# Optimization experiments

Measured on AMD Instinct MI355X. Metric: run time of the kernel, lower is better.

The kernel has to match this reference:

```python
import jax, jax.numpy as jnp
import numpy as np

N_HEADS = 16
EPS = 1e-5

def _ln(h, g, b):
    mu = jnp.mean(h, axis=-1, keepdims=True)
    var = jnp.var(h, axis=-1, keepdims=True)
    return (h - mu) * jax.lax.rsqrt(var + EPS) * g + b

def setup_inputs() -> dict:
    key = jax.random.key(0)
    ks = jax.random.split(key, 8)
    B, S, D, M = 2, 2048, 2048, 8192
    x = jax.random.normal(ks[0], (B, S, D), dtype=jnp.float32)
    # causal mask: True where attention is disallowed (j > i)
    mask = jnp.triu(jnp.ones((S, S), dtype=bool), k=1)[None, None]
    s = 1.0 / np.sqrt(D)
    Wq = jax.random.normal(ks[1], (D, D), dtype=jnp.float32) * s
    Wk = jax.random.normal(ks[2], (D, D), dtype=jnp.float32) * s
    Wv = jax.random.normal(ks[3], (D, D), dtype=jnp.float32) * s
    Wo = jax.random.normal(ks[4], (D, D), dtype=jnp.float32) * s
    W1 = jax.random.normal(ks[5], (D, M), dtype=jnp.float32) * s
    b1 = jnp.zeros((M,), dtype=jnp.float32)
    W2 = jax.random.normal(ks[6], (M, D), dtype=jnp.float32) * (1.0 / np.sqrt(M))
    b2 = jnp.zeros((D,), dtype=jnp.float32)
    ln1_g = jnp.ones((D,), jnp.float32); ln1_b = jnp.zeros((D,), jnp.float32)
    ln2_g = jnp.ones((D,), jnp.float32); ln2_b = jnp.zeros((D,), jnp.float32)
    return dict(x=x, self_attn_mask=mask, Wq=Wq, Wk=Wk, Wv=Wv, Wo=Wo,
                ln1_g=ln1_g, ln1_b=ln1_b, W1=W1, b1=b1, W2=W2, b2=b2,
                ln2_g=ln2_g, ln2_b=ln2_b)

def reference(x, self_attn_mask, Wq, Wk, Wv, Wo, ln1_g, ln1_b, W1, b1, W2, b2, ln2_g, ln2_b):
    B, S, D = x.shape
    n = N_HEADS
    d = D // n
    # --- self-attention with pre-norm residual ---
    h = _ln(x, ln1_g, ln1_b)
    # NOTE: source uses .view(b, n_heads, i, head_dim) with NO transpose -> plain reshape
    q = (h @ Wq).reshape(B, n, S, d)
    k = (h @ Wk).reshape(B, n, S, d)
    v = (h @ Wv).reshape(B, n, S, d)
    score = jnp.einsum('bnid,bnjd->bnij', q, k)
    # NOTE: source masks BEFORE scaling, so -1e9 is also divided by sqrt(d)
    score = jnp.where(self_attn_mask, jnp.float32(-1e9), score) / jnp.sqrt(jnp.float32(d))
    w = jax.nn.softmax(score, axis=3)
    o = jnp.einsum('bnij,bnjd->bnid', w, v)
    o = o.transpose(0, 2, 1, 3).reshape(B, S, D)  # b n i d -> b i (n d)
    x = x + o @ Wo
    # --- FFN with pre-norm residual ---
    h2 = _ln(x, ln2_g, ln2_b)
    ff = jnp.maximum(h2 @ W1 + b1, 0.0) @ W2 + b2
    return x + ff
```

## Files before the change

### kernel.cpp

```cpp
#include <hip/hip_runtime.h>
#include <cstdint>

using bf16x8 = __attribute__((ext_vector_type(8))) short;
using f32x4  = __attribute__((ext_vector_type(4))) float;

__device__ __forceinline__ unsigned short f2bf(float f) {
  union { float f; unsigned u; } v; v.f = f;
  unsigned u = v.u;
  u += 0x7fffu + ((u >> 16) & 1u);
  return (unsigned short)(u >> 16);
}

__global__ __launch_bounds__(256) void ln_kernel(
    const float* __restrict__ x, const float* __restrict__ g,
    const float* __restrict__ bb, unsigned short* __restrict__ h)
{
  const int D = 2048;
  const int row = blockIdx.x;
  const float* xr = x + (size_t)row * D;
  const int t = threadIdx.x;
  float4 v0 = ((const float4*)xr)[t];
  float4 v1 = ((const float4*)xr)[t + 256];
  float s  = v0.x+v0.y+v0.z+v0.w + v1.x+v1.y+v1.z+v1.w;
  float ss = v0.x*v0.x+v0.y*v0.y+v0.z*v0.z+v0.w*v0.w
           + v1.x*v1.x+v1.y*v1.y+v1.z*v1.z+v1.w*v1.w;
  #pragma unroll
  for (int off = 1; off < 64; off <<= 1) {
    s  += __shfl_xor(s, off);
    ss += __shfl_xor(ss, off);
  }
  __shared__ float red[8];
  const int wave = t >> 6, lane = t & 63;
  if (lane == 0) { red[wave] = s; red[4+wave] = ss; }
  __syncthreads();
  s  = red[0]+red[1]+red[2]+red[3];
  ss = red[4]+red[5]+red[6]+red[7];
  const float mu   = s * (1.f/2048.f);
  const float var  = ss * (1.f/2048.f) - mu*mu;
  const float rstd = rsqrtf(var + 1e-5f);
  unsigned short* hr = h + (size_t)row * D;
  #pragma unroll
  for (int q = 0; q < 2; ++q) {
    float4 v = q ? v1 : v0;
    int vecidx = t + q*256;
    float4 gg  = ((const float4*)g)[vecidx];
    float4 bv  = ((const float4*)bb)[vecidx];
    ushort4 o;
    o.x = f2bf((v.x-mu)*rstd*gg.x + bv.x);
    o.y = f2bf((v.y-mu)*rstd*gg.y + bv.y);
    o.z = f2bf((v.z-mu)*rstd*gg.z + bv.z);
    o.w = f2bf((v.w-mu)*rstd*gg.w + bv.w);
    *(ushort4*)(hr + vecidx*4) = o;
  }
}

__global__ __launch_bounds__(256) void transpose_cast(
    const float* __restrict__ W, unsigned short* __restrict__ WT,
    int K, int N)
{
  __shared__ float tile[32][33];
  const int tx = threadIdx.x, ty = threadIdx.y;
  const int n0 = blockIdx.x * 32, k0 = blockIdx.y * 32;
  #pragma unroll
  for (int r = 0; r < 4; ++r)
    tile[ty + r*8][tx] = W[(size_t)(k0 + ty + r*8) * N + n0 + tx];
  __syncthreads();
  #pragma unroll
  for (int r = 0; r < 4; ++r)
    WT[(size_t)(n0 + ty + r*8) * K + k0 + tx] = f2bf(tile[tx][ty + r*8]);
}

template<bool BIAS, bool RELU, bool RESID, bool OUTBF16>
__global__ __launch_bounds__(256, 2) void gemm_bt(
    const unsigned short* __restrict__ A, const unsigned short* __restrict__ BT,
    const float* __restrict__ bias, const float* __restrict__ resid,
    void* __restrict__ Cp, int M, int N, int K)
{
  constexpr int BM = 128, BN = 128, BK = 64, PK = 72;
  __shared__ __align__(16) unsigned short As[BM*PK];
  __shared__ __align__(16) unsigned short Bs[BN*PK];
  const int tid  = threadIdx.x;
  const int lane = tid & 63;
  const int wave = tid >> 6;
  const int l15 = lane & 15, lh = lane >> 4;
  const size_t bm = (size_t)blockIdx.y * BM, bn = (size_t)blockIdx.x * BN;
  const int wm = (wave >> 1) * 64, wn = (wave & 1) * 64;
  f32x4 acc[4][4] = {};
  bf16x8 ar[4], br[4];
  const int nk = K / BK;

  auto loadG = [&](int kt) {
    #pragma unroll
    for (int q = 0; q < 4; ++q) {
      int c = tid + q*256;
      int row = c >> 3, k0 = (c & 7) * 8;
      ar[q] = *(const bf16x8*)(A  + (bm + row)*(size_t)K + (size_t)kt*BK + k0);
      br[q] = *(const bf16x8*)(BT + (bn + row)*(size_t)K + (size_t)kt*BK + k0);
    }
  };
  loadG(0);
  for (int kt = 0; kt < nk; ++kt) {
    __syncthreads();
    #pragma unroll
    for (int q = 0; q < 4; ++q) {
      int c = tid + q*256;
      int row = c >> 3, k0 = (c & 7) * 8;
      *(bf16x8*)(&As[row*PK + k0]) = ar[q];
      *(bf16x8*)(&Bs[row*PK + k0]) = br[q];
    }
    __syncthreads();
    if (kt + 1 < nk) loadG(kt + 1);
    #pragma unroll
    for (int kk = 0; kk < 2; ++kk) {
      bf16x8 af[4], bfr[4];
      #pragma unroll
      for (int i = 0; i < 4; ++i) {
        af[i]  = *(const bf16x8*)(&As[(wm + i*16 + l15)*PK + kk*32 + lh*8]);
        bfr[i] = *(const bf16x8*)(&Bs[(wn + i*16 + l15)*PK + kk*32 + lh*8]);
      }
      #pragma unroll
      for (int i = 0; i < 4; ++i)
        #pragma unroll
        for (int j = 0; j < 4; ++j)
          acc[i][j] = __builtin_amdgcn_mfma_f32_16x16x32_bf16(af[i], bfr[j], acc[i][j], 0, 0, 0);
    }
  }
  float bv[4];
  if (BIAS) {
    #pragma unroll
    for (int j = 0; j < 4; ++j) bv[j] = bias[bn + wn + j*16 + l15];
  }
  #pragma unroll
  for (int i = 0; i < 4; ++i) {
    #pragma unroll
    for (int r = 0; r < 4; ++r) {
      size_t rrow = bm + wm + i*16 + lh*4 + r;
      #pragma unroll
      for (int j = 0; j < 4; ++j) {
        size_t ccol = bn + wn + j*16 + l15;
        float v = acc[i][j][r];
        if (BIAS)  v += bv[j];
        if (RELU)  v = fmaxf(v, 0.f);
        if (RESID) v += resid[rrow*(size_t)N + ccol];
        if (OUTBF16) ((unsigned short*)Cp)[rrow*(size_t)N + ccol] = f2bf(v);
        else         ((float*)Cp)[rrow*(size_t)N + ccol] = v;
      }
    }
  }
}

__global__ __launch_bounds__(256) void attn_kernel(
    const unsigned short* __restrict__ QKV, unsigned short* __restrict__ O)
{
  constexpr float SCALE = 0.08838834764831845f;
  __shared__ __align__(16) unsigned short Kl[64*128];
  __shared__ __align__(16) unsigned short Vf[64*128];
  __shared__ __align__(16) unsigned short Pl[4*1024];
  const int bid = blockIdx.x;
  const int qt = 31 - (bid >> 5);
  const int nh = bid & 15;
  const int b  = (bid >> 4) & 1;
  const int t = threadIdx.x;
  const int lane = t & 63, wave = t >> 6;
  const int l15 = lane & 15, lh = lane >> 4;
  const int i0 = qt*64 + wave*16;
  const size_t RS = 6144;
  const size_t base = (size_t)b * 2048 * RS;

  const unsigned short* qrow = QKV + base + (size_t)(nh*128 + (i0 >> 4)) * RS;
  bf16x8 qf[4];
  #pragma unroll
  for (int c = 0; c < 4; ++c)
    qf[c] = *(const bf16x8*)(qrow + l15*128 + c*32 + lh*8);

  f32x4 of[8] = {};
  float mrun[4], lrun[4];
  #pragma unroll
  for (int r = 0; r < 4; ++r) { mrun[r] = -INFINITY; lrun[r] = 0.f; }

  const int nkt = qt + 1;
  bf16x8 kr[4], vr[4];
  auto loadKV = [&](int kt) {
    #pragma unroll
    for (int q = 0; q < 4; ++q) {
      int c = t + q*256;
      int j = c >> 4, dd0 = (c & 15) * 8;
      const size_t grow = base + (size_t)(nh*128 + kt*4 + (j >> 4)) * RS + (j & 15)*128 + dd0;
      kr[q] = *(const bf16x8*)(QKV + grow + 2048);
      vr[q] = *(const bf16x8*)(QKV + grow + 4096);
    }
  };
  loadKV(0);

  for (int kt = 0; kt < nkt; ++kt) {
    __syncthreads();
    #pragma unroll
    for (int q = 0; q < 4; ++q) {
      int c = t + q*256;
      int j = c >> 4, dd0 = (c & 15) * 8;
      *(bf16x8*)((char*)Kl + ((j*256 + dd0*2) ^ ((j & 7) << 4))) = kr[q];
      int ks = j >> 5, jq = j & 31;
      int cc = dd0 >> 4;
      int wb = ks*8192 + cc*1024 + (((dd0 & 15) + 16*((jq >> 3) & 3)) & ~7)*16 + (jq & 7)*2;
      #pragma unroll
      for (int e = 0; e < 8; ++e)
        *(unsigned short*)((char*)Vf + wb + ((e ^ cc) * 16)) = (unsigned short)vr[q][e];
    }
    __syncthreads();
    if (kt + 1 < nkt) loadKV(kt + 1);

    f32x4 sc[4] = {};
    #pragma unroll
    for (int jt = 0; jt < 4; ++jt) {
      int row = jt*16 + l15;
      const char* kb = (const char*)Kl + row*256;
      const int sw = (row & 7) << 4;
      #pragma unroll
      for (int c = 0; c < 4; ++c) {
        bf16x8 kf = *(const bf16x8*)(kb + ((c*64 + lh*16) ^ sw));
        sc[jt] = __builtin_amdgcn_mfma_f32_16x16x32_bf16(qf[c], kf, sc[jt], 0, 0, 0);
      }
    }

    float fac[4];
    char* pw = (char*)Pl + wave*2048;
    #pragma unroll
    for (int r = 0; r < 4; ++r) {
      float s0 = sc[0][r]*SCALE, s1 = sc[1][r]*SCALE, s2 = sc[2][r]*SCALE, s3 = sc[3][r]*SCALE;
      if (kt == qt) {
        const int i = i0 + lh*4 + r;
        const int j = kt*64 + l15;
        s0 = (j      > i) ? -INFINITY : s0;
        s1 = (j + 16 > i) ? -INFINITY : s1;
        s2 = (j + 32 > i) ? -INFINITY : s2;
        s3 = (j + 48 > i) ? -INFINITY : s3;
      }
      float mx = fmaxf(fmaxf(s0, s1), fmaxf(s2, s3));
      #pragma unroll
      for (int mk = 1; mk < 16; mk <<= 1) mx = fmaxf(mx, __shfl_xor(mx, mk));
      const float mnew = fmaxf(mrun[r], mx);
      float p0 = __expf(s0 - mnew), p1 = __expf(s1 - mnew);
      float p2 = __expf(s2 - mnew), p3 = __expf(s3 - mnew);
      float psum = (p0 + p1) + (p2 + p3);
      #pragma unroll
      for (int mk = 1; mk < 16; mk <<= 1) psum += __shfl_xor(psum, mk);
      fac[r]  = __expf(mrun[r] - mnew);
      lrun[r] = lrun[r]*fac[r] + psum;
      mrun[r] = mnew;
      const int io = lh*4 + r;
      const int swp = (io & 7) << 4;
      char* pr = pw + io*128;
      *(unsigned short*)(pr + ((     l15*2) ^ swp)) = f2bf(p0);
      *(unsigned short*)(pr + ((32 + l15*2) ^ swp)) = f2bf(p1);
      *(unsigned short*)(pr + ((64 + l15*2) ^ swp)) = f2bf(p2);
      *(unsigned short*)(pr + ((96 + l15*2) ^ swp)) = f2bf(p3);
    }
    #pragma unroll
    for (int c = 0; c < 8; ++c)
      #pragma unroll
      for (int r = 0; r < 4; ++r)
        of[c][r] *= fac[r];

    const char* prd = pw + l15*128;
    const int psw = (l15 & 7) << 4;
    bf16x8 pa0 = *(const bf16x8*)(prd + ((     lh*16) ^ psw));
    bf16x8 pa1 = *(const bf16x8*)(prd + ((64 + lh*16) ^ psw));

    #pragma unroll
    for (int c = 0; c < 8; ++c) {
      const char* vb = (const char*)Vf + c*1024 + ((lane ^ c) * 16);
      bf16x8 v0 = *(const bf16x8*)(vb);
      bf16x8 v1 = *(const bf16x8*)(vb + 8192);
      of[c] = __builtin_amdgcn_mfma_f32_16x16x32_bf16(pa0, v0, of[c], 0, 0, 0);
      of[c] = __builtin_amdgcn_mfma_f32_16x16x32_bf16(pa1, v1, of[c], 0, 0, 0);
    }
  }

  unsigned short* orow = O + ((size_t)(b*2048 + i0))*2048 + nh*128;
  #pragma unroll
  for (int r = 0; r < 4; ++r) {
    const float inv = 1.f / lrun[r];
    #pragma unroll
    for (int c = 0; c < 8; ++c)
      orow[(size_t)(lh*4 + r)*2048 + c*16 + l15] = f2bf(of[c][r]*inv);
  }
}

extern "C" void kernel_launch(void* const* d_in, const int* in_sizes, int n_in,
                              void* d_out, int out_size, void* d_ws, size_t ws_size,
                              hipStream_t stream)
{
  const float* x    = (const float*)d_in[0];
  const float* Wq   = (const float*)d_in[2];
  const float* Wk   = (const float*)d_in[3];
  const float* Wv   = (const float*)d_in[4];
  const float* Wo   = (const float*)d_in[5];
  const float* ln1g = (const float*)d_in[6];
  const float* ln1b = (const float*)d_in[7];
  const float* W1   = (const float*)d_in[8];
  const float* b1   = (const float*)d_in[9];
  const float* W2   = (const float*)d_in[10];
  const float* b2   = (const float*)d_in[11];
  const float* ln2g = (const float*)d_in[12];
  const float* ln2b = (const float*)d_in[13];
  float* out = (float*)d_out;

  char* ws = (char*)d_ws;
  unsigned short* WqkvT  = (unsigned short*)(ws);
  unsigned short* WoT    = (unsigned short*)(ws + 25165824);
  unsigned short* W1T    = (unsigned short*)(ws + 33554432);
  unsigned short* W2T    = (unsigned short*)(ws + 67108864);
  unsigned short* h      = (unsigned short*)(ws + 100663296);
  float*          x2     = (float*)(ws + 117440512);
  unsigned short* QKV    = (unsigned short*)(ws + 150994944);
  unsigned short* attn_o = (unsigned short*)(ws + 201326592);
  unsigned short* ff1    = (unsigned short*)(ws + 150994944);

  dim3 tb(32, 8);
  transpose_cast<<<dim3(64, 64),  tb, 0, stream>>>(Wq, WqkvT,                2048, 2048);
  transpose_cast<<<dim3(64, 64),  tb, 0, stream>>>(Wk, WqkvT + 2048*2048,    2048, 2048);
  transpose_cast<<<dim3(64, 64),  tb, 0, stream>>>(Wv, WqkvT + 2*2048*2048,  2048, 2048);
  transpose_cast<<<dim3(64, 64),  tb, 0, stream>>>(Wo, WoT,                  2048, 2048);
  transpose_cast<<<dim3(256, 64), tb, 0, stream>>>(W1, W1T,                  2048, 8192);
  transpose_cast<<<dim3(64, 256), tb, 0, stream>>>(W2, W2T,                  8192, 2048);

  ln_kernel<<<4096, 256, 0, stream>>>(x, ln1g, ln1b, h);
  gemm_bt<false,false,false,true><<<dim3(48, 32), 256, 0, stream>>>(
      h, WqkvT, nullptr, nullptr, QKV, 4096, 6144, 2048);
  attn_kernel<<<1024, 256, 0, stream>>>(QKV, attn_o);
  gemm_bt<false,false,true,false><<<dim3(16, 32), 256, 0, stream>>>(
      attn_o, WoT, nullptr, x, x2, 4096, 2048, 2048);
  ln_kernel<<<4096, 256, 0, stream>>>(x2, ln2g, ln2b, h);
  gemm_bt<true,true,false,true><<<dim3(64, 32), 256, 0, stream>>>(
      h, W1T, b1, nullptr, ff1, 4096, 8192, 2048);
  gemm_bt<true,false,true,false><<<dim3(16, 32), 256, 0, stream>>>(
      ff1, W2T, b2, x2, out, 4096, 2048, 8192);
}
```

Measured before the change: 674.6 us.

## Replace GEMM with 256-row tiles, direct global-to-LDS double-buffered loads

Rewrites the bf16 GEMM to use 512-thread blocks with 256xBN tiles and double-buffered LDS. Tiles are filled by direct global_load_lds with an XOR swizzle in place of the register-staged, padded layout. A workgroup index swizzle is added for L2 locality, and MFMA phases are interleaved with barriers and raised s_setprio. The goal is to hide global load latency, raise per-block data reuse, and cut register traffic, at the cost of larger LDS use per block and fewer blocks for the N=2048 GEMMs.

```diff
diff --git a/kernel.cpp b/kernel.cpp
--- a/kernel.cpp
+++ b/kernel.cpp
@@ -9,6 +9,12 @@
   unsigned u = v.u;
   u += 0x7fffu + ((u >> 16) & 1u);
   return (unsigned short)(u >> 16);
+}
+
+__device__ __forceinline__ void gload_lds16(const unsigned short* g, unsigned short* l) {
+  __builtin_amdgcn_global_load_lds(
+      (const __attribute__((address_space(1))) unsigned int*)g,
+      (__attribute__((address_space(3))) unsigned int*)l, 16, 0, 0);
 }
 
 __global__ __launch_bounds__(256) void ln_kernel(
@@ -70,76 +76,125 @@
     WT[(size_t)(n0 + ty + r*8) * K + k0 + tx] = f2bf(tile[tx][ty + r*8]);
 }
 
-template<bool BIAS, bool RELU, bool RESID, bool OUTBF16>
-__global__ __launch_bounds__(256, 2) void gemm_bt(
+template<int BN, bool BIAS, bool RELU, bool RESID, bool OUTBF16>
+__global__ __launch_bounds__(512, 2) void gemm8(
     const unsigned short* __restrict__ A, const unsigned short* __restrict__ BT,
     const float* __restrict__ bias, const float* __restrict__ resid,
-    void* __restrict__ Cp, int M, int N, int K)
-{
-  constexpr int BM = 128, BN = 128, BK = 64, PK = 72;
-  __shared__ __align__(16) unsigned short As[BM*PK];
-  __shared__ __align__(16) unsigned short Bs[BN*PK];
+    void* __restrict__ Cp, int M, int N, int K, int nbx)
+{
+  constexpr int BM = 256, BK = 64;
+  constexpr int NREP = BN / 64;
+  constexpr int BLD  = BN / 64;
+  constexpr int LPK  = 4 + BLD;
+  __shared__ __align__(16) unsigned short lds[2][(BM + BN) * BK];
+
   const int tid  = threadIdx.x;
-  const int lane = tid & 63;
-  const int wave = tid >> 6;
+  const int lane = tid & 63, wave = tid >> 6;
   const int l15 = lane & 15, lh = lane >> 4;
-  const size_t bm = (size_t)blockIdx.y * BM, bn = (size_t)blockIdx.x * BN;
-  const int wm = (wave >> 1) * 64, wn = (wave & 1) * 64;
-  f32x4 acc[4][4] = {};
-  bf16x8 ar[4], br[4];
-  const int nk = K / BK;
-
-  auto loadG = [&](int kt) {
-    #pragma unroll
-    for (int q = 0; q < 4; ++q) {
-      int c = tid + q*256;
-      int row = c >> 3, k0 = (c & 7) * 8;
-      ar[q] = *(const bf16x8*)(A  + (bm + row)*(size_t)K + (size_t)kt*BK + k0);
-      br[q] = *(const bf16x8*)(BT + (bn + row)*(size_t)K + (size_t)kt*BK + k0);
+  const int wr = wave >> 2, wc = wave & 3;
+
+  const int nwg = gridDim.x;
+  const int q8  = nwg >> 3;
+  const int wg  = blockIdx.x;
+  const int swz = (wg & 7) * q8 + (wg >> 3);
+  const size_t bm = (size_t)(swz / nbx) * BM;
+  const size_t bn = (size_t)(swz % nbx) * BN;
+
+  const int nk = K >> 6;
+
+  auto stage = [&](int buf, int kt) {
+    unsigned short* La = &lds[buf][0];
+    unsigned short* Lb = &lds[buf][BM * BK];
+    #pragma unroll
+    for (int qq = 0; qq < 4; ++qq) {
+      int idx = qq * 512 + tid;
+      int row = idx >> 3, c = idx & 7;
+      int gc = c ^ (row & 7);
+      gload_lds16(A + (bm + row) * (size_t)K + (size_t)kt * BK + gc * 8,
+                  La + idx * 8);
+    }
+    #pragma unroll
+    for (int qq = 0; qq < BLD; ++qq) {
+      int idx = qq * 512 + tid;
+      int row = idx >> 3, c = idx & 7;
+      int gc = c ^ (row & 7);
+      gload_lds16(BT + (bn + row) * (size_t)K + (size_t)kt * BK + gc * 8,
+                  Lb + idx * 8);
     }
   };
-  loadG(0);
+
+  f32x4 acc[8][NREP] = {};
+
+  stage(0, 0);
+  stage(1, 1);
+
   for (int kt = 0; kt < nk; ++kt) {
-    __syncthreads();
-    #pragma unroll
-    for (int q = 0; q < 4; ++q) {
-      int c = tid + q*256;
-      int row = c >> 3, k0 = (c & 7) * 8;
-      *(bf16x8*)(&As[row*PK + k0]) = ar[q];
-      *(bf16x8*)(&Bs[row*PK + k0]) = br[q];
-    }
-    __syncthreads();
-    if (kt + 1 < nk) loadG(kt + 1);
-    #pragma unroll
-    for (int kk = 0; kk < 2; ++kk) {
-      bf16x8 af[4], bfr[4];
-      #pragma unroll
-      for (int i = 0; i < 4; ++i) {
-        af[i]  = *(const bf16x8*)(&As[(wm + i*16 + l15)*PK + kk*32 + lh*8]);
-        bfr[i] = *(const bf16x8*)(&Bs[(wn + i*16 + l15)*PK + kk*32 + lh*8]);
-      }
-      #pragma unroll
-      for (int i = 0; i < 4; ++i)
+    const int buf = kt & 1;
+    if (kt < nk - 1) {
+      asm volatile("s_waitcnt vmcnt(%0)" :: "i"(LPK) : "memory");
+    } else {
+      asm volatile("s_waitcnt vmcnt(0)" ::: "memory");
+    }
+    __builtin_amdgcn_s_barrier();
+    asm volatile("" ::: "memory");
+
+    const unsigned short* La = &lds[buf][0];
+    const unsigned short* Lb = &lds[buf][BM * BK];
+    bf16x8 bfr[2][NREP];
+    #pragma unroll
+    for (int p = 0; p < 4; ++p) {
+      if (p == 0) {
         #pragma unroll
-        for (int j = 0; j < 4; ++j)
-          acc[i][j] = __builtin_amdgcn_mfma_f32_16x16x32_bf16(af[i], bfr[j], acc[i][j], 0, 0, 0);
-    }
-  }
-  float bv[4];
+        for (int kk = 0; kk < 2; ++kk)
+          #pragma unroll
+          for (int n = 0; n < NREP; ++n) {
+            int brow = wc * (BN / 4) + n * 16 + l15;
+            bfr[kk][n] = *(const bf16x8*)(Lb + brow * 64 +
+                           ((kk * 32 + lh * 8) ^ ((brow & 7) << 3)));
+          }
+      }
+      bf16x8 af[2][2];
+      #pragma unroll
+      for (int mi = 0; mi < 2; ++mi) {
+        int arow = wr * 128 + (p * 2 + mi) * 16 + l15;
+        #pragma unroll
+        for (int kk = 0; kk < 2; ++kk)
+          af[mi][kk] = *(const bf16x8*)(La + arow * 64 +
+                         ((kk * 32 + lh * 8) ^ ((arow & 7) << 3)));
+      }
+      asm volatile("" ::: "memory");
+      __builtin_amdgcn_s_barrier();
+      __builtin_amdgcn_s_setprio(1);
+      #pragma unroll
+      for (int mi = 0; mi < 2; ++mi)
+        #pragma unroll
+        for (int n = 0; n < NREP; ++n)
+          #pragma unroll
+          for (int kk = 0; kk < 2; ++kk)
+            acc[p*2+mi][n] = __builtin_amdgcn_mfma_f32_16x16x32_bf16(
+                af[mi][kk], bfr[kk][n], acc[p*2+mi][n], 0, 0, 0);
+      __builtin_amdgcn_s_setprio(0);
+      asm volatile("" ::: "memory");
+      __builtin_amdgcn_s_barrier();
+    }
+    if (kt + 2 < nk) stage(buf, kt + 2);
+  }
+
+  float bv[NREP];
   if (BIAS) {
     #pragma unroll
-    for (int j = 0; j < 4; ++j) bv[j] = bias[bn + wn + j*16 + l15];
-  }
-  #pragma unroll
-  for (int i = 0; i < 4; ++i) {
+    for (int n = 0; n < NREP; ++n) bv[n] = bias[bn + wc*(BN/4) + n*16 + l15];
+  }
+  #pragma unroll
+  for (int m = 0; m < 8; ++m) {
     #pragma unroll
     for (int r = 0; r < 4; ++r) {
-      size_t rrow = bm + wm + i*16 + lh*4 + r;
-      #pragma unroll
-      for (int j = 0; j < 4; ++j) {
-        size_t ccol = bn + wn + j*16 + l15;
-        float v = acc[i][j][r];
-        if (BIAS)  v += bv[j];
+      size_t rrow = bm + wr*128 + m*16 + lh*4 + r;
+      #pragma unroll
+      for (int n = 0; n < NREP; ++n) {
+        size_t ccol = bn + wc*(BN/4) + n*16 + l15;
+        float v = acc[m][n][r];
+        if (BIAS)  v += bv[n];
         if (RELU)  v = fmaxf(v, 0.f);
         if (RESID) v += resid[rrow*(size_t)N + ccol];
         if (OUTBF16) ((unsigned short*)Cp)[rrow*(size_t)N + ccol] = f2bf(v);
@@ -325,14 +380,14 @@
   transpose_cast<<<dim3(64, 256), tb, 0, stream>>>(W2, W2T,                  8192, 2048);
 
   ln_kernel<<<4096, 256, 0, stream>>>(x, ln1g, ln1b, h);
-  gemm_bt<false,false,false,true><<<dim3(48, 32), 256, 0, stream>>>(
-      h, WqkvT, nullptr, nullptr, QKV, 4096, 6144, 2048);
+  gemm8<256,false,false,false,true><<<384, 512, 0, stream>>>(
+      h, WqkvT, nullptr, nullptr, QKV, 4096, 6144, 2048, 24);
   attn_kernel<<<1024, 256, 0, stream>>>(QKV, attn_o);
-  gemm_bt<false,false,true,false><<<dim3(16, 32), 256, 0, stream>>>(
-      attn_o, WoT, nullptr, x, x2, 4096, 2048, 2048);
+  gemm8<128,false,false,true,false><<<256, 512, 0, stream>>>(
+      attn_o, WoT, nullptr, x, x2, 4096, 2048, 2048, 16);
   ln_kernel<<<4096, 256, 0, stream>>>(x2, ln2g, ln2b, h);
-  gemm_bt<true,true,false,true><<<dim3(64, 32), 256, 0, stream>>>(
-      h, W1T, b1, nullptr, ff1, 4096, 8192, 2048);
-  gemm_bt<true,false,true,false><<<dim3(16, 32), 256, 0, stream>>>(
-      ff1, W2T, b2, x2, out, 4096, 2048, 8192);
-}
+  gemm8<256,true,true,false,true><<<512, 512, 0, stream>>>(
+      h, W1T, b1, nullptr, ff1, 4096, 8192, 2048, 32);
+  gemm8<128,true,false,true,false><<<256, 512, 0, stream>>>(
+      ff1, W2T, b2, x2, out, 4096, 2048, 8192, 16);
+}
```

Result: faster. 647.9 us (-4.0%).
